# Optimization experiments

Measured on AMD Instinct MI355X. Metric: run time of the kernel, lower is better.

## Reference

```python
import jax, jax.numpy as jnp
import numpy as np

N = 3072
SIGMA = 1.0
NORM_FACTOR = 90.4756
TWOPI = 2.0 * np.pi
NORM_CONST = NORM_FACTOR / TWOPI
A = 1.0 / (SIGMA * 2.0 ** 0.5)
SQRT_PI = np.pi ** 0.5


def setup_inputs() -> dict:
    key = jax.random.key(0)
    ks = jax.random.split(key, 6)
    q = jax.random.normal(ks[0], (N,), dtype=jnp.float32)
    r = jax.random.uniform(ks[1], (N, 3), dtype=jnp.float32) * 30.0  # 30A box
    cell = jnp.zeros((1, 3, 3), dtype=jnp.float32)  # det<1e-6 -> realspace path
    batch = jnp.zeros((N,), dtype=jnp.int32)
    u = jax.random.normal(ks[2], (N, 3), dtype=jnp.float32)
    kappa = jax.random.uniform(ks[3], (N,), dtype=jnp.float32)
    alpha = jax.random.uniform(ks[4], (N,), dtype=jnp.float32)
    return {"q": q, "r": r, "cell": cell, "batch": batch, "u": u, "kappa": kappa, "alpha": alpha}


def _ewald_realspace(q, r, u, kappa, alpha):
    # q:[n], r:[n,3], u:[n,3], kappa:[n], alpha:[n]; single batch, n_q=1 path
    n = q.shape[0]
    eye = jnp.eye(n, dtype=r.dtype)
    off = 1.0 - eye  # mask_off
    r_ij = r[None, :, :] - r[:, None, :]            # [n,n,3], r_j - r_i
    d2 = jnp.sum(r_ij * r_ij, axis=-1)
    rnorm = jnp.sqrt(d2 + eye)                      # diag padded with 1 for grad safety
    rinv = off / rnorm                              # 0 on diagonal
    rinv2 = rinv * rinv
    rinv3 = rinv2 * rinv
    erf = jax.scipy.special.erf(rnorm * A) * off    # 0 on diagonal
    gauss = jnp.exp(-(A * rnorm) ** 2) * off

    # charge-charge
    f_qq = erf * rinv * NORM_CONST
    e_phi = jnp.einsum('i,ij->j', q, f_qq)
    pot = 0.5 * jnp.dot(e_phi, q)

    # dipole kernels
    s1 = erf * rinv3 - (2.0 * A / SQRT_PI) * gauss * rinv2
    s2 = 3.0 * erf * rinv3 - (6.0 * A / SQRT_PI) * gauss * rinv2 - (4.0 * A ** 3 / SQRT_PI) * gauss

    # charge-dipole: f_qu[i,j,c] = s1[i,j]*r_ij[i,j,c]*NORM_CONST (contracted on the fly)
    ur = jnp.einsum('ic,ijc->ij', u, r_ij)          # u_i . r_ij
    e_phi_u = NORM_CONST * jnp.einsum('ij,ij->j', s1, ur)
    e_phi = e_phi + e_phi_u
    pot = pot + jnp.dot(e_phi_u, q)

    # dipole-dipole: f_uu = NORM_CONST*(s2 * rhat rhat^T - s1 * I), contracted without [n,n,3,3]
    rhat = r_ij * rinv[..., None]
    ai = jnp.einsum('ic,ijc->ij', u, rhat)          # u_i . rhat_ij
    bj = jnp.einsum('jc,ijc->ij', u, rhat)          # u_j . rhat_ij
    uu = u @ u.T
    pot = pot - 0.5 * NORM_CONST * (jnp.sum(s2 * ai * bj) - jnp.sum(s1 * uu))

    # induced charges (remove_self_interaction=True: no self terms)
    q_induced = -kappa * e_phi
    pot = pot + 0.5 * jnp.dot(e_phi, q_induced)

    # electric field (alpha is not None -> computed)
    e_field = NORM_CONST * jnp.einsum('i,ij,ijc->jc', q, s1, r_ij)
    E_u = NORM_CONST * (jnp.einsum('ij,ijd->jd', s2 * ai, rhat) - s1.T @ u)
    e_field = e_field + E_u

    # induced dipoles (alpha scalar per node)
    u_induced = e_field * alpha[:, None]
    pot = pot - 0.5 * jnp.sum(e_field * u_induced)

    return pot.reshape(1), q_induced, u_induced


def reference(q, r, cell, batch, u, kappa, alpha):
    # cell is zeros (det < 1e-6) and batch is all-zeros -> single-system realspace branch
    return _ewald_realspace(q, r, u, kappa, alpha)
```

## Files before the change

kernel.cpp:

```cpp
#include <hip/hip_runtime.h>

#define NATOMS 3072
#define CHUNKS 16
#define WPB 4
#define IPB (NATOMS / CHUNKS)
#define IPW (IPB / WPB)
#define PPW (IPW / 2)

static_assert(IPB * CHUNKS == NATOMS, "i-partition must cover all atoms");
static_assert(IPW * WPB == IPB, "wave split must cover block chunk");
static_assert((IPW & 1) == 0, "packed loop needs even IPW");
static_assert((IPB & 1) == 0, "pair-SoA staging needs even IPB");

constexpr float NCf = (float)(90.4756 / (2.0 * 3.14159265358979323846));
constexpr float Af = 0.70710678118654752f;
constexpr float Cf = 0.79788456080286536f;

typedef float v2f __attribute__((ext_vector_type(2)));

__device__ __forceinline__ v2f vfma(v2f a, v2f b, v2f c) {
  return __builtin_elementwise_fma(a, b, c);
}
__device__ __forceinline__ v2f splat(float x) {
  v2f v; v.x = x; v.y = x; return v;
}
__device__ __forceinline__ v2f lo2(float4 f) { v2f v; v.x = f.x; v.y = f.y; return v; }
__device__ __forceinline__ v2f hi2(float4 f) { v2f v; v.x = f.z; v.y = f.w; return v; }

template <bool DIAG>
__device__ __forceinline__ void pair_loop(
    const float4* __restrict__ sPU, int p0, int jt,
    float pjx, float pjy, float pjz,
    v2f& acc0, v2f& acc1, v2f& acc2, v2f& acc3,
    v2f& acc4, v2f& acc5, v2f& acc6, v2f& acc7) {
#pragma unroll 2
  for (int p = p0; p < p0 + PPW; ++p) {
    const float4 f0 = sPU[4 * p + 0];
    const float4 f1 = sPU[4 * p + 1];
    const float4 f2 = sPU[4 * p + 2];
    const float4 f3 = sPU[4 * p + 3];
    const v2f pix = lo2(f0), piy = hi2(f0);
    const v2f piz = lo2(f1), qi  = hi2(f1);
    const v2f uix = lo2(f2), uiy = hi2(f2);
    const v2f uiz = lo2(f3);

    const v2f dx = splat(pjx) - pix;
    const v2f dy = splat(pjy) - piy;
    const v2f dz = splat(pjz) - piz;
    v2f d2 = vfma(dx, dx, vfma(dy, dy, dz * dz));
    if (DIAG) {
      if (2 * p == jt)     d2.x = 1e18f;
      if (2 * p + 1 == jt) d2.y = 1e18f;
    }

    v2f rinv;
    rinv.x = __builtin_amdgcn_rsqf(d2.x);
    rinv.y = __builtin_amdgcn_rsqf(d2.y);
    const v2f rinv2 = rinv * rinv;
    const v2f rinv3 = rinv2 * rinv;
    const v2f ur = vfma(uix, dx, vfma(uiy, dy, uiz * dz));

    v2f e0, s1, s2;
    if (__any(fminf(d2.x, d2.y) < 18.0f)) {
      const v2f rnorm = d2 * rinv;
      v2f g0;
      g0.x = __expf(-0.5f * d2.x);
      g0.y = __expf(-0.5f * d2.y);
      v2f tt;
      tt.x = __builtin_amdgcn_rcpf(fmaf(0.3275911f * Af, rnorm.x, 1.0f));
      tt.y = __builtin_amdgcn_rcpf(fmaf(0.3275911f * Af, rnorm.y, 1.0f));
      const v2f poly =
          tt * vfma(tt,
                    vfma(tt,
                         vfma(tt,
                              vfma(tt, splat(1.061405429f),
                                   splat(-1.453152027f)),
                              splat(1.421413741f)),
                         splat(-0.284496736f)),
                    splat(0.254829592f));
      const v2f erfv = vfma(-poly, g0, splat(1.0f));
      const v2f cg = splat(Cf) * g0;
      e0 = erfv * rinv;
      s1 = erfv * rinv3 - cg * rinv2;
      s2 = vfma(splat(3.0f), s1, -cg);
    } else {
      e0 = rinv;
      s1 = rinv3;
      s2 = splat(3.0f) * rinv3;
    }

    acc0 = vfma(qi, e0, acc0);
    acc1 = vfma(s1, ur, acc1);
    const v2f qs1 = qi * s1;
    acc2 = vfma(qs1, dx, acc2);
    acc3 = vfma(qs1, dy, acc3);
    acc4 = vfma(qs1, dz, acc4);
    const v2f t2 = s2 * ur * rinv2;
    acc5 = vfma(t2, dx, vfma(-s1, uix, acc5));
    acc6 = vfma(t2, dy, vfma(-s1, uiy, acc6));
    acc7 = vfma(t2, dz, vfma(-s1, uiz, acc7));
  }
}

__global__ __launch_bounds__(256)
void ewald_main(const float* __restrict__ q, const float* __restrict__ r,
                const float* __restrict__ u, float* __restrict__ part,
                float* __restrict__ out) {
  const int lane = threadIdx.x & 63;
  const int w = threadIdx.x >> 6;
  const int j = blockIdx.x * 64 + lane;

  if (blockIdx.x == 0 && blockIdx.y == 0 && threadIdx.x == 0) out[0] = 0.0f;

  __shared__ float4 sPU[2 * IPB];
  const int i0 = blockIdx.y * IPB;
  for (int p = threadIdx.x; p < IPB / 2; p += 256) {
    const int ia = i0 + 2 * p, ib = ia + 1;
    sPU[4 * p + 0] = make_float4(r[3 * ia + 0], r[3 * ib + 0],
                                 r[3 * ia + 1], r[3 * ib + 1]);
    sPU[4 * p + 1] = make_float4(r[3 * ia + 2], r[3 * ib + 2], q[ia], q[ib]);
    sPU[4 * p + 2] = make_float4(u[3 * ia + 0], u[3 * ib + 0],
                                 u[3 * ia + 1], u[3 * ib + 1]);
    sPU[4 * p + 3] = make_float4(u[3 * ia + 2], u[3 * ib + 2], 0.f, 0.f);
  }
  const float pjx = r[3 * j + 0];
  const float pjy = r[3 * j + 1];
  const float pjz = r[3 * j + 2];
  __syncthreads();

  v2f acc0 = splat(0.f), acc1 = splat(0.f), acc2 = splat(0.f),
      acc3 = splat(0.f), acc4 = splat(0.f), acc5 = splat(0.f),
      acc6 = splat(0.f), acc7 = splat(0.f);

  const int jt = j - i0;
  const int p0 = w * PPW;

  const int jlo = blockIdx.x * 64;
  const bool diagW = (jlo - i0 < 2 * p0 + IPW) && (2 * p0 < jlo - i0 + 64);
  if (diagW)
    pair_loop<true>(sPU, p0, jt, pjx, pjy, pjz,
                    acc0, acc1, acc2, acc3, acc4, acc5, acc6, acc7);
  else
    pair_loop<false>(sPU, p0, jt, pjx, pjy, pjz,
                     acc0, acc1, acc2, acc3, acc4, acc5, acc6, acc7);

  float a0 = acc0.x + acc0.y, a1 = acc1.x + acc1.y;
  float a2 = acc2.x + acc2.y, a3 = acc3.x + acc3.y;
  float a4 = acc4.x + acc4.y, a5 = acc5.x + acc5.y;
  float a6 = acc6.x + acc6.y, a7 = acc7.x + acc7.y;

  __shared__ float red[(WPB - 1) * 64 * 8];
  if (w > 0) {
    float* dst = &red[((w - 1) * 64 + lane) * 8];
    dst[0] = a0; dst[1] = a1; dst[2] = a2; dst[3] = a3;
    dst[4] = a4; dst[5] = a5; dst[6] = a6; dst[7] = a7;
  }
  __syncthreads();
  if (w == 0) {
#pragma unroll
    for (int ww = 0; ww < WPB - 1; ++ww) {
      const float* src = &red[(ww * 64 + lane) * 8];
      a0 += src[0]; a1 += src[1]; a2 += src[2]; a3 += src[3];
      a4 += src[4]; a5 += src[5]; a6 += src[6]; a7 += src[7];
    }
    float4* dst = (float4*)&part[((size_t)blockIdx.y * NATOMS + j) * 8];
    dst[0] = make_float4(a0, a1, a2, a3);
    dst[1] = make_float4(a4, a5, a6, a7);
  }
}

__global__ __launch_bounds__(256)
void ewald_finalize(const float* __restrict__ part, const float* __restrict__ q,
                    const float* __restrict__ u, const float* __restrict__ kappa,
                    const float* __restrict__ alpha, float* __restrict__ out) {
  const int j = blockIdx.x * blockDim.x + threadIdx.x;

  float s[8] = {0.f, 0.f, 0.f, 0.f, 0.f, 0.f, 0.f, 0.f};
#pragma unroll
  for (int c = 0; c < CHUNKS; ++c) {
    const float4* src = (const float4*)&part[((size_t)c * NATOMS + j) * 8];
    const float4 a = src[0];
    const float4 b = src[1];
    s[0] += a.x; s[1] += a.y; s[2] += a.z; s[3] += a.w;
    s[4] += b.x; s[5] += b.y; s[6] += b.z; s[7] += b.w;
  }

  const float e_phi = NCf * (s[0] + s[1]);
  const float Eux = NCf * s[5];
  const float Euy = NCf * s[6];
  const float Euz = NCf * s[7];
  const float efx = NCf * s[2] + Eux;
  const float efy = NCf * s[3] + Euy;
  const float efz = NCf * s[4] + Euz;

  const float qj = q[j];
  const float kj = kappa[j];
  const float aj = alpha[j];
  const float ujx = u[3 * j + 0];
  const float ujy = u[3 * j + 1];
  const float ujz = u[3 * j + 2];

  out[1 + j] = -kj * e_phi;
  out[1 + NATOMS + 3 * j + 0] = aj * efx;
  out[1 + NATOMS + 3 * j + 1] = aj * efy;
  out[1 + NATOMS + 3 * j + 2] = aj * efz;

  float potj = 0.5f * NCf * s[0] * qj
             + NCf * s[1] * qj
             - 0.5f * (ujx * Eux + ujy * Euy + ujz * Euz)
             - 0.5f * kj * e_phi * e_phi
             - 0.5f * aj * (efx * efx + efy * efy + efz * efz);

#pragma unroll
  for (int m = 32; m >= 1; m >>= 1) potj += __shfl_xor(potj, m, 64);
  __shared__ float lred[4];
  const int lane = threadIdx.x & 63;
  const int wid = threadIdx.x >> 6;
  if (lane == 0) lred[wid] = potj;
  __syncthreads();
  if (threadIdx.x == 0) {
    atomicAdd(out, lred[0] + lred[1] + lred[2] + lred[3]);
  }
}

extern "C" void kernel_launch(void* const* d_in, const int* in_sizes, int n_in,
                              void* d_out, int out_size, void* d_ws,
                              size_t ws_size, hipStream_t stream) {
  const float* q = (const float*)d_in[0];
  const float* r = (const float*)d_in[1];
  const float* u = (const float*)d_in[4];
  const float* kappa = (const float*)d_in[5];
  const float* alpha = (const float*)d_in[6];
  float* out = (float*)d_out;

  float* part = (float*)d_ws;

  ewald_main<<<dim3(NATOMS / 64, CHUNKS), 256, 0, stream>>>(q, r, u, part, out);
  ewald_finalize<<<dim3(NATOMS / 256), 256, 0, stream>>>(part, q, u, kappa,
                                                         alpha, out);
}
```

Measured before the change: 79.59 us.

## Fuse finalize into main kernel via global ticket spin-wait

Merges the two kernel launches into one. Each block publishes its partial sums, fences, and increments a global ticket, and the first FBLOCKS blocks spin until every block has arrived before doing the finalize reduction. This removes the second launch and its gap but adds a memset, an atomic per block, and a grid-wide spin that relies on all 768 blocks being co-resident or able to progress. Blocks 0..11 wait while holding CUs, and out[0] zeroing by block 0 could race with other blocks' atomicAdd.

```diff
diff --git a/kernel.cpp b/kernel.cpp
--- a/kernel.cpp
+++ b/kernel.cpp
@@ -6,6 +6,8 @@
 #define IPB (NATOMS / CHUNKS)
 #define IPW (IPB / WPB)
 #define PPW (IPW / 2)
+#define NBLOCKS ((NATOMS / 64) * CHUNKS)
+#define FBLOCKS (NATOMS / 256)
 
 static_assert(IPB * CHUNKS == NATOMS, "i-partition must cover all atoms");
 static_assert(IPW * WPB == IPB, "wave split must cover block chunk");
@@ -103,9 +105,10 @@
 }
 
 __global__ __launch_bounds__(256)
-void ewald_main(const float* __restrict__ q, const float* __restrict__ r,
-                const float* __restrict__ u, float* __restrict__ part,
-                float* __restrict__ out) {
+void ewald_fused(const float* __restrict__ q, const float* __restrict__ r,
+                 const float* __restrict__ u, const float* __restrict__ kappa,
+                 const float* __restrict__ alpha, float* __restrict__ part,
+                 unsigned int* __restrict__ ticket, float* __restrict__ out) {
   const int lane = threadIdx.x & 63;
   const int w = threadIdx.x >> 6;
   const int j = blockIdx.x * 64 + lane;
@@ -166,19 +169,27 @@
     float4* dst = (float4*)&part[((size_t)blockIdx.y * NATOMS + j) * 8];
     dst[0] = make_float4(a0, a1, a2, a3);
     dst[1] = make_float4(a4, a5, a6, a7);
-  }
-}
-
-__global__ __launch_bounds__(256)
-void ewald_finalize(const float* __restrict__ part, const float* __restrict__ q,
-                    const float* __restrict__ u, const float* __restrict__ kappa,
-                    const float* __restrict__ alpha, float* __restrict__ out) {
-  const int j = blockIdx.x * blockDim.x + threadIdx.x;
+    __threadfence();
+  }
+  __syncthreads();
+  if (threadIdx.x == 0) atomicAdd(ticket, 1u);
+
+  const int bid = blockIdx.y * gridDim.x + blockIdx.x;
+  if (bid >= FBLOCKS) return;
+
+  if (threadIdx.x == 0) {
+    while (__hip_atomic_load(ticket, __ATOMIC_ACQUIRE,
+                             __HIP_MEMORY_SCOPE_AGENT) < (unsigned)NBLOCKS)
+      __builtin_amdgcn_s_sleep(2);
+  }
+  __syncthreads();
+
+  const int jf = bid * 256 + threadIdx.x;
 
   float s[8] = {0.f, 0.f, 0.f, 0.f, 0.f, 0.f, 0.f, 0.f};
 #pragma unroll
   for (int c = 0; c < CHUNKS; ++c) {
-    const float4* src = (const float4*)&part[((size_t)c * NATOMS + j) * 8];
+    const float4* src = (const float4*)&part[((size_t)c * NATOMS + jf) * 8];
     const float4 a = src[0];
     const float4 b = src[1];
     s[0] += a.x; s[1] += a.y; s[2] += a.z; s[3] += a.w;
@@ -193,17 +204,17 @@
   const float efy = NCf * s[3] + Euy;
   const float efz = NCf * s[4] + Euz;
 
-  const float qj = q[j];
-  const float kj = kappa[j];
-  const float aj = alpha[j];
-  const float ujx = u[3 * j + 0];
-  const float ujy = u[3 * j + 1];
-  const float ujz = u[3 * j + 2];
-
-  out[1 + j] = -kj * e_phi;
-  out[1 + NATOMS + 3 * j + 0] = aj * efx;
-  out[1 + NATOMS + 3 * j + 1] = aj * efy;
-  out[1 + NATOMS + 3 * j + 2] = aj * efz;
+  const float qj = q[jf];
+  const float kj = kappa[jf];
+  const float aj = alpha[jf];
+  const float ujx = u[3 * jf + 0];
+  const float ujy = u[3 * jf + 1];
+  const float ujz = u[3 * jf + 2];
+
+  out[1 + jf] = -kj * e_phi;
+  out[1 + NATOMS + 3 * jf + 0] = aj * efx;
+  out[1 + NATOMS + 3 * jf + 1] = aj * efy;
+  out[1 + NATOMS + 3 * jf + 2] = aj * efz;
 
   float potj = 0.5f * NCf * s[0] * qj
              + NCf * s[1] * qj
@@ -214,9 +225,7 @@
 #pragma unroll
   for (int m = 32; m >= 1; m >>= 1) potj += __shfl_xor(potj, m, 64);
   __shared__ float lred[4];
-  const int lane = threadIdx.x & 63;
-  const int wid = threadIdx.x >> 6;
-  if (lane == 0) lred[wid] = potj;
+  if (lane == 0) lred[w] = potj;
   __syncthreads();
   if (threadIdx.x == 0) {
     atomicAdd(out, lred[0] + lred[1] + lred[2] + lred[3]);
@@ -234,8 +243,11 @@
   float* out = (float*)d_out;
 
   float* part = (float*)d_ws;
-
-  ewald_main<<<dim3(NATOMS / 64, CHUNKS), 256, 0, stream>>>(q, r, u, part, out);
-  ewald_finalize<<<dim3(NATOMS / 256), 256, 0, stream>>>(part, q, u, kappa,
-                                                         alpha, out);
-}
+  unsigned int* ticket =
+      (unsigned int*)((char*)d_ws + (size_t)CHUNKS * NATOMS * 8 * sizeof(float));
+
+  hipMemsetAsync(ticket, 0, sizeof(unsigned int), stream);
+
+  ewald_fused<<<dim3(NATOMS / 64, CHUNKS), 256, 0, stream>>>(
+      q, r, u, kappa, alpha, part, ticket, out);
+}
```

Measured after the change: 96.55 us. 21.3% more time.
